# Kernel tuning notes

Hardware: AMD Instinct MI355X
Metric: run time of the kernel (lower is better)

## Reference

```python
import jax, jax.numpy as jnp
from jax import lax
import numpy as np

INPUT_DIM = 64
EMB_DIM = 24   # hardcoded Dense(24) in MyLSTM
UNITS = 128    # hardcoded LSTM_cell(128)


def setup_inputs() -> dict:
    key = jax.random.key(0)
    ks = jax.random.split(key, 12)
    B, T, D = 1024, 2048, INPUT_DIM
    gin = EMB_DIM + UNITS  # 152: concat([x_emb, h])
    s_emb = 1.0 / np.sqrt(D)
    s_g = 1.0 / np.sqrt(gin)
    s_o = 1.0 / np.sqrt(UNITS)
    return {
        "x": jax.random.normal(ks[0], (B, T, D), jnp.float32),
        "W_emb": jax.random.normal(ks[1], (D, EMB_DIM), jnp.float32) * s_emb,
        "b_emb": jnp.zeros((EMB_DIM,), jnp.float32),
        "Wf": jax.random.normal(ks[2], (gin, UNITS), jnp.float32) * s_g,
        "bf": jnp.ones((UNITS,), jnp.float32),  # forget bias init = ones
        "Wi": jax.random.normal(ks[3], (gin, UNITS), jnp.float32) * s_g,
        "bi": jnp.zeros((UNITS,), jnp.float32),
        "Wg": jax.random.normal(ks[4], (gin, UNITS), jnp.float32) * s_g,
        "bg": jnp.zeros((UNITS,), jnp.float32),
        "Wo": jax.random.normal(ks[5], (gin, UNITS), jnp.float32) * s_g,
        "bo": jnp.zeros((UNITS,), jnp.float32),
        "W_out": jax.random.normal(ks[6], (UNITS, 1), jnp.float32) * s_o,
        "b_out": jnp.zeros((1,), jnp.float32),
    }


def reference(x, W_emb, b_emb, Wf, bf, Wi, bi, Wg, bg, Wo, bo, W_out, b_out):
    # embedding: Dense(24, sigmoid) applied per timestep
    e = jax.nn.sigmoid(jnp.einsum("btd,de->bte", x, W_emb) + b_emb)  # [B,T,24]
    B = x.shape[0]
    h0 = jnp.zeros((B, UNITS), x.dtype)
    c0 = jnp.zeros((B, UNITS), x.dtype)

    def step(carry, xt):
        h, c = carry
        z = jnp.concatenate([xt, h], axis=-1)  # [B, 152]
        f = jax.nn.sigmoid(z @ Wf + bf)
        i = jax.nn.sigmoid(z @ Wi + bi)
        g = jnp.tanh(z @ Wg + bg)
        o = jax.nn.sigmoid(z @ Wo + bo)
        c_new = c * f + i * g
        h_new = jnp.tanh(c_new) * o
        return (h_new, c_new), None

    (h_last, _), _ = lax.scan(step, (h0, c0), jnp.swapaxes(e, 0, 1))  # scan over T
    return jax.nn.sigmoid(h_last @ W_out + b_out)  # [B, 1]
```

## Files before the change

kernel.cpp:

```cpp
#include <hip/hip_runtime.h>
#include <hip/hip_bf16.h>

#define T_STEPS 2048
#define BATCH   1024
#define NUNITS  128
#define ROWS    4
#define LOG2E   1.4426950408889634f

typedef __attribute__((ext_vector_type(4))) float  f32x4;
typedef __attribute__((ext_vector_type(2))) int    i32x2;
typedef __attribute__((ext_vector_type(4))) int    int4v;

__device__ __forceinline__ float sigm_pre(float xs) {
    return __builtin_amdgcn_rcpf(1.0f + __builtin_amdgcn_exp2f(-xs));
}
__device__ __forceinline__ float tanh_pre(float xs) {
    return fmaf(-2.0f, __builtin_amdgcn_rcpf(1.0f + __builtin_amdgcn_exp2f(xs)), 1.0f);
}
__device__ __forceinline__ int swap_lo_i(int a, int b) {
    i32x2 r = __builtin_amdgcn_permlane32_swap(a, b, false, false);
    return r[0];
}
__device__ __forceinline__ int swap16_lo_i(int a, int b) {
    i32x2 r = __builtin_amdgcn_permlane16_swap(a, b, false, false);
    return r[0];
}

__global__ __launch_bounds__(256) void emb_kernel(const float* __restrict__ x,
                                                  const float* __restrict__ Wemb,
                                                  const float* __restrict__ bemb,
                                                  uchar* __restrict__ e_out) {
    int g = blockIdx.x * 256 + threadIdx.x;
    int t = g >> 10;
    int b = g & 1023;
    const float* xr = x + ((size_t)b * T_STEPS + t) * 64;

    float4 xv[16];
#pragma unroll
    for (int i = 0; i < 16; i++) xv[i] = ((const float4*)xr)[i];

    float acc[24];
#pragma unroll
    for (int j = 0; j < 24; j++) acc[j] = bemb[j];

#pragma unroll
    for (int d = 0; d < 64; d++) {
        float xs = ((const float*)xv)[d];
#pragma unroll
        for (int j = 0; j < 24; j++) acc[j] = fmaf(xs, Wemb[d * 24 + j], acc[j]);
    }

    uint outp[8] = {0, 0, 0, 0, 0, 0, 0, 0};
#pragma unroll
    for (int j = 0; j < 24; j++) {
        float s = __builtin_amdgcn_rcpf(1.0f + __builtin_amdgcn_exp2f(-LOG2E * acc[j]));
        int q = (int)__builtin_rintf(s * 127.0f);
        outp[j >> 2] |= (uint)(q & 255) << (8 * (j & 3));
    }
    uint4* dst = (uint4*)(e_out + (size_t)g * 32);
    dst[0] = ((const uint4*)outp)[0];
    dst[1] = ((const uint4*)outp)[1];
}

__global__ __launch_bounds__(512, 1) void lstm_kernel(
    const uchar* __restrict__ e_ws,
    const float* __restrict__ Wf, const float* __restrict__ bf_,
    const float* __restrict__ Wi, const float* __restrict__ bi_,
    const float* __restrict__ Wg, const float* __restrict__ bg_,
    const float* __restrict__ Wo, const float* __restrict__ bo_,
    const float* __restrict__ Wout, const float* __restrict__ bout,
    float* __restrict__ out) {
    __shared__ __align__(16) char zq[2][2][4][16][16];

    const int tid  = threadIdx.x;
    const int lane = tid & 63;
    const int wv   = tid >> 6;
    const int l15  = lane & 15;
    const int kg   = lane >> 4;
    const int r0   = blockIdx.x * ROWS;

    const float* Wp[4] = {Wf, Wi, Wg, Wo};
    const float* Bp[4] = {bf_, bi_, bg_, bo_};
    const float gsc[4] = {LOG2E, LOG2E, 2.0f * LOG2E, LOG2E};
    const int ucol = wv * 16 + l15;

    int4v wq[4][3];
    float fct[4], biasv[4];
#pragma unroll
    for (int gt = 0; gt < 4; gt++) {
        float amax = 1e-20f;
        for (int k = 0; k < 152; k++) {
            float v = (k < 128) ? Wp[gt][(24 + k) * NUNITS + ucol]
                                : Wp[gt][(k - 128) * NUNITS + ucol];
            amax = fmaxf(amax, fabsf(v * gsc[gt]));
        }
        float isq = 127.0f / amax;
        fct[gt] = amax * (1.0f / 16129.0f);
#pragma unroll
        for (int ks = 0; ks < 3; ks++) {
#pragma unroll
            for (int w = 0; w < 4; w++) {
                int word = 0;
#pragma unroll
                for (int b = 0; b < 4; b++) {
                    int k = ks * 64 + kg * 16 + w * 4 + b;
                    float v = 0.0f;
                    if (k < 128) v = Wp[gt][(24 + k) * NUNITS + ucol] * gsc[gt];
                    else if (k < 152) v = Wp[gt][(k - 128) * NUNITS + ucol] * gsc[gt];
                    int q = (int)__builtin_rintf(v * isq);
                    word |= (q & 255) << (8 * b);
                }
                wq[gt][ks][w] = word;
            }
        }
        biasv[gt] = Bp[gt][ucol] * gsc[gt];
    }
    const int4v zeroi = {0, 0, 0, 0};

    for (int i = tid; i < (int)(sizeof(zq) / 4); i += 512) ((int*)zq)[i] = 0;

    const char* zrd = &zq[0][0][kg][l15][0];
    char* zwr = &zq[0][ucol >> 6][(ucol >> 4) & 3][kg][ucol & 15];

    const uchar* elbase = e_ws + ((size_t)(r0 + (l15 & 3)) * 32 + kg * 16);
    const bool eload = (kg < 2) && (l15 < 4);
    int4v e0 = zeroi, e1 = zeroi;
    if (eload) {
        e0 = *(const int4v*)(const void*)(elbase);
        e1 = *(const int4v*)(const void*)(elbase + 32768);
    }
    const uchar* eptr = elbase + 2 * 32768;

    __syncthreads();

    float c0 = 0.0f;

    auto STEP = [&](int P, int4v& ecur) {
        int4v acc[4];
#pragma unroll
        for (int gt = 0; gt < 4; gt++)
            acc[gt] = __builtin_amdgcn_mfma_i32_16x16x64_i8(ecur, wq[gt][2], zeroi, 0, 0, 0);

        const char* zb = zrd + P * 2048;
        int4v z0 = *(const int4v*)(const void*)(zb);
        int4v z1 = *(const int4v*)(const void*)(zb + 1024);
#pragma unroll
        for (int gt = 0; gt < 4; gt++)
            acc[gt] = __builtin_amdgcn_mfma_i32_16x16x64_i8(z0, wq[gt][0], acc[gt], 0, 0, 0);
#pragma unroll
        for (int gt = 0; gt < 4; gt++)
            acc[gt] = __builtin_amdgcn_mfma_i32_16x16x64_i8(z1, wq[gt][1], acc[gt], 0, 0, 0);

        if (eload) ecur = *(const int4v*)(const void*)(eptr);
        eptr += 32768;

        float g[4];
#pragma unroll
        for (int gt = 0; gt < 4; gt++) {
            int a0 = swap_lo_i(acc[gt][0], acc[gt][2]);
            int a1 = swap_lo_i(acc[gt][1], acc[gt][3]);
            int sel = swap16_lo_i(a0, a1);
            g[gt] = fmaf((float)sel, fct[gt], biasv[gt]);
        }

        float fg = sigm_pre(g[0]);
        float ig = sigm_pre(g[1]);
        float gg = tanh_pre(g[2]);
        float og = sigm_pre(g[3]);
        c0 = fmaf(c0, fg, ig * gg);
        float h0 = tanh_pre(2.0f * LOG2E * c0) * og;

        int q0i = (int)__builtin_rintf(h0 * 127.0f);
        *(zwr + ((P ^ 1) * 2048)) = (char)q0i;

        asm volatile("s_waitcnt lgkmcnt(0)" ::: "memory");
        __builtin_amdgcn_s_barrier();
        __builtin_amdgcn_sched_barrier(0);
    };

    for (int t = 0; t < T_STEPS; t += 2) {
        STEP(0, e0);
        STEP(1, e1);
    }

    if (tid < ROWS) {
        float s2 = 0.0f;
#pragma unroll
        for (int k = 0; k < NUNITS; k++)
            s2 += (float)zq[0][k >> 6][(k >> 4) & 3][tid][k & 15] * Wout[k];
        float s = s2 * (1.0f / 127.0f) + bout[0];
        out[r0 + tid] = __builtin_amdgcn_rcpf(1.0f + __builtin_amdgcn_exp2f(-LOG2E * s));
    }
}

extern "C" void kernel_launch(void* const* d_in, const int* in_sizes, int n_in,
                              void* d_out, int out_size, void* d_ws, size_t ws_size,
                              hipStream_t stream) {
    const float* x     = (const float*)d_in[0];
    const float* Wemb  = (const float*)d_in[1];
    const float* bemb  = (const float*)d_in[2];
    const float* Wf    = (const float*)d_in[3];
    const float* bf_   = (const float*)d_in[4];
    const float* Wi    = (const float*)d_in[5];
    const float* bi_   = (const float*)d_in[6];
    const float* Wg    = (const float*)d_in[7];
    const float* bg_   = (const float*)d_in[8];
    const float* Wo    = (const float*)d_in[9];
    const float* bo_   = (const float*)d_in[10];
    const float* Wout  = (const float*)d_in[11];
    const float* bout  = (const float*)d_in[12];
    float* out = (float*)d_out;
    uchar* e_ws = (uchar*)d_ws;

    int nrows = BATCH * T_STEPS;
    emb_kernel<<<nrows / 256, 256, 0, stream>>>(x, Wemb, bemb, e_ws);
    lstm_kernel<<<BATCH / ROWS, 512, 0, stream>>>(e_ws, Wf, bf_, Wi, bi_, Wg, bg_,
                                                  Wo, bo_, Wout, bout, out);
}
```

Before: 1.214 ms.

## Run one batch row per single-wave block to eliminate per-step barriers

Each batch row now gets its own single-wave block instead of eight waves sharing four rows. Each lane keeps all 8×4 quantized weight tiles in registers and computes every gate tile itself. The workgroup s_barrier in each recurrent step is gone, and the hidden-state LDS buffer is reduced to single buffering. The cost is about four times more MFMA work per useful row, since only one of the 16 MFMA rows carries real data. It also adds very high register pressure from the 96 int4 weight vectors and leaves fewer waves per CU.

```diff
diff --git a/kernel.cpp b/kernel.cpp
--- a/kernel.cpp
+++ b/kernel.cpp
@@ -4,10 +4,8 @@
 #define T_STEPS 2048
 #define BATCH   1024
 #define NUNITS  128
-#define ROWS    4
 #define LOG2E   1.4426950408889634f
 
-typedef __attribute__((ext_vector_type(4))) float  f32x4;
 typedef __attribute__((ext_vector_type(2))) int    i32x2;
 typedef __attribute__((ext_vector_type(4))) int    int4v;
 
@@ -62,7 +60,7 @@
     dst[1] = ((const uint4*)outp)[1];
 }
 
-__global__ __launch_bounds__(512, 1) void lstm_kernel(
+__global__ __launch_bounds__(64) void lstm_kernel(
     const uchar* __restrict__ e_ws,
     const float* __restrict__ Wf, const float* __restrict__ bf_,
     const float* __restrict__ Wi, const float* __restrict__ bi_,
@@ -70,60 +68,81 @@
     const float* __restrict__ Wo, const float* __restrict__ bo_,
     const float* __restrict__ Wout, const float* __restrict__ bout,
     float* __restrict__ out) {
-    __shared__ __align__(16) char zq[2][2][4][16][16];
-
-    const int tid  = threadIdx.x;
-    const int lane = tid & 63;
-    const int wv   = tid >> 6;
+    __shared__ __align__(16) char zq[2][4][16][16];
+
+    const int lane = threadIdx.x & 63;
     const int l15  = lane & 15;
     const int kg   = lane >> 4;
-    const int r0   = blockIdx.x * ROWS;
+    const int r0   = blockIdx.x;
 
     const float* Wp[4] = {Wf, Wi, Wg, Wo};
     const float* Bp[4] = {bf_, bi_, bg_, bo_};
     const float gsc[4] = {LOG2E, LOG2E, 2.0f * LOG2E, LOG2E};
-    const int ucol = wv * 16 + l15;
-
-    int4v wq[4][3];
-    float fct[4], biasv[4];
-#pragma unroll
-    for (int gt = 0; gt < 4; gt++) {
-        float amax = 1e-20f;
-        for (int k = 0; k < 152; k++) {
-            float v = (k < 128) ? Wp[gt][(24 + k) * NUNITS + ucol]
-                                : Wp[gt][(k - 128) * NUNITS + ucol];
-            amax = fmaxf(amax, fabsf(v * gsc[gt]));
-        }
-        float isq = 127.0f / amax;
-        fct[gt] = amax * (1.0f / 16129.0f);
-#pragma unroll
-        for (int ks = 0; ks < 3; ks++) {
-#pragma unroll
-            for (int w = 0; w < 4; w++) {
-                int word = 0;
-#pragma unroll
-                for (int b = 0; b < 4; b++) {
-                    int k = ks * 64 + kg * 16 + w * 4 + b;
-                    float v = 0.0f;
-                    if (k < 128) v = Wp[gt][(24 + k) * NUNITS + ucol] * gsc[gt];
-                    else if (k < 152) v = Wp[gt][(k - 128) * NUNITS + ucol] * gsc[gt];
-                    int q = (int)__builtin_rintf(v * isq);
-                    word |= (q & 255) << (8 * b);
+
+    const int Ta = (kg & 1) + ((kg >> 1) << 2);
+    const int Tb = Ta + 2;
+    const int ua = Ta * 16 + l15, ub = Tb * 16 + l15;
+
+    int4v wq[8][4][3];
+#pragma unroll
+    for (int T = 0; T < 8; T++) {
+        const int ucol = T * 16 + l15;
+#pragma unroll
+        for (int gt = 0; gt < 4; gt++) {
+            float amax = 1e-20f;
+            for (int k = 0; k < 152; k++) {
+                float v = (k < 128) ? Wp[gt][(24 + k) * NUNITS + ucol]
+                                    : Wp[gt][(k - 128) * NUNITS + ucol];
+                amax = fmaxf(amax, fabsf(v * gsc[gt]));
+            }
+            float isq = 127.0f / amax;
+#pragma unroll
+            for (int ks = 0; ks < 3; ks++) {
+#pragma unroll
+                for (int w = 0; w < 4; w++) {
+                    int word = 0;
+#pragma unroll
+                    for (int b = 0; b < 4; b++) {
+                        int k = ks * 64 + kg * 16 + w * 4 + b;
+                        float v = 0.0f;
+                        if (k < 128) v = Wp[gt][(24 + k) * NUNITS + ucol] * gsc[gt];
+                        else if (k < 152) v = Wp[gt][(k - 128) * NUNITS + ucol] * gsc[gt];
+                        int q = (int)__builtin_rintf(v * isq);
+                        word |= (q & 255) << (8 * b);
+                    }
+                    wq[T][gt][ks][w] = word;
                 }
-                wq[gt][ks][w] = word;
             }
         }
-        biasv[gt] = Bp[gt][ucol] * gsc[gt];
+    }
+    float fct_a[4], fct_b[4], bias_a[4], bias_b[4];
+#pragma unroll
+    for (int gt = 0; gt < 4; gt++) {
+        float ama = 1e-20f, amb = 1e-20f;
+        for (int k = 0; k < 152; k++) {
+            float va = (k < 128) ? Wp[gt][(24 + k) * NUNITS + ua]
+                                 : Wp[gt][(k - 128) * NUNITS + ua];
+            float vb = (k < 128) ? Wp[gt][(24 + k) * NUNITS + ub]
+                                 : Wp[gt][(k - 128) * NUNITS + ub];
+            ama = fmaxf(ama, fabsf(va * gsc[gt]));
+            amb = fmaxf(amb, fabsf(vb * gsc[gt]));
+        }
+        fct_a[gt] = ama * (1.0f / 16129.0f);
+        fct_b[gt] = amb * (1.0f / 16129.0f);
+        bias_a[gt] = Bp[gt][ua] * gsc[gt];
+        bias_b[gt] = Bp[gt][ub] * gsc[gt];
     }
     const int4v zeroi = {0, 0, 0, 0};
 
-    for (int i = tid; i < (int)(sizeof(zq) / 4); i += 512) ((int*)zq)[i] = 0;
-
-    const char* zrd = &zq[0][0][kg][l15][0];
-    char* zwr = &zq[0][ucol >> 6][(ucol >> 4) & 3][kg][ucol & 15];
-
-    const uchar* elbase = e_ws + ((size_t)(r0 + (l15 & 3)) * 32 + kg * 16);
-    const bool eload = (kg < 2) && (l15 < 4);
+    for (int i = lane; i < (int)(sizeof(zq) / 4); i += 64) ((int*)zq)[i] = 0;
+
+    const char* zr0 = &zq[0][kg][l15][0];
+    const char* zr1 = &zq[1][kg][l15][0];
+    char* wa = &zq[ua >> 6][(ua >> 4) & 3][0][ua & 15];
+    char* wb = &zq[ub >> 6][(ub >> 4) & 3][0][ub & 15];
+
+    const uchar* elbase = e_ws + ((size_t)r0 * 32 + kg * 16);
+    const bool eload = (kg < 2) && (l15 == 0);
     int4v e0 = zeroi, e1 = zeroi;
     if (eload) {
         e0 = *(const int4v*)(const void*)(elbase);
@@ -133,63 +152,67 @@
 
     __syncthreads();
 
-    float c0 = 0.0f;
-
-    auto STEP = [&](int P, int4v& ecur) {
-        int4v acc[4];
-#pragma unroll
-        for (int gt = 0; gt < 4; gt++)
-            acc[gt] = __builtin_amdgcn_mfma_i32_16x16x64_i8(ecur, wq[gt][2], zeroi, 0, 0, 0);
-
-        const char* zb = zrd + P * 2048;
-        int4v z0 = *(const int4v*)(const void*)(zb);
-        int4v z1 = *(const int4v*)(const void*)(zb + 1024);
-#pragma unroll
-        for (int gt = 0; gt < 4; gt++)
-            acc[gt] = __builtin_amdgcn_mfma_i32_16x16x64_i8(z0, wq[gt][0], acc[gt], 0, 0, 0);
-#pragma unroll
-        for (int gt = 0; gt < 4; gt++)
-            acc[gt] = __builtin_amdgcn_mfma_i32_16x16x64_i8(z1, wq[gt][1], acc[gt], 0, 0, 0);
+    float ca = 0.0f, cb = 0.0f;
+
+    auto STEP = [&](int4v& ecur) {
+        int4v z0 = *(const int4v*)(const void*)(zr0);
+        int4v z1 = *(const int4v*)(const void*)(zr1);
+
+        float gA[4], gB[4];
+#pragma unroll
+        for (int gt = 0; gt < 4; gt++) {
+            int4v acc[8];
+#pragma unroll
+            for (int T = 0; T < 8; T++)
+                acc[T] = __builtin_amdgcn_mfma_i32_16x16x64_i8(ecur, wq[T][gt][2], zeroi, 0, 0, 0);
+#pragma unroll
+            for (int T = 0; T < 8; T++)
+                acc[T] = __builtin_amdgcn_mfma_i32_16x16x64_i8(z0, wq[T][gt][0], acc[T], 0, 0, 0);
+#pragma unroll
+            for (int T = 0; T < 8; T++)
+                acc[T] = __builtin_amdgcn_mfma_i32_16x16x64_i8(z1, wq[T][gt][1], acc[T], 0, 0, 0);
+
+            int s0 = swap_lo_i(acc[0][0], acc[4][0]);
+            int s1 = swap_lo_i(acc[1][0], acc[5][0]);
+            int s2 = swap_lo_i(acc[2][0], acc[6][0]);
+            int s3 = swap_lo_i(acc[3][0], acc[7][0]);
+            int va = swap16_lo_i(s0, s1);
+            int vb = swap16_lo_i(s2, s3);
+            gA[gt] = fmaf((float)va, fct_a[gt], bias_a[gt]);
+            gB[gt] = fmaf((float)vb, fct_b[gt], bias_b[gt]);
+        }
 
         if (eload) ecur = *(const int4v*)(const void*)(eptr);
         eptr += 32768;
 
-        float g[4];
-#pragma unroll
-        for (int gt = 0; gt < 4; gt++) {
-            int a0 = swap_lo_i(acc[gt][0], acc[gt][2]);
-            int a1 = swap_lo_i(acc[gt][1], acc[gt][3]);
-            int sel = swap16_lo_i(a0, a1);
-            g[gt] = fmaf((float)sel, fct[gt], biasv[gt]);
-        }
-
-        float fg = sigm_pre(g[0]);
-        float ig = sigm_pre(g[1]);
-        float gg = tanh_pre(g[2]);
-        float og = sigm_pre(g[3]);
-        c0 = fmaf(c0, fg, ig * gg);
-        float h0 = tanh_pre(2.0f * LOG2E * c0) * og;
-
-        int q0i = (int)__builtin_rintf(h0 * 127.0f);
-        *(zwr + ((P ^ 1) * 2048)) = (char)q0i;
+        float fga = sigm_pre(gA[0]), fgb = sigm_pre(gB[0]);
+        float iga = sigm_pre(gA[1]), igb = sigm_pre(gB[1]);
+        float gga = tanh_pre(gA[2]), ggb = tanh_pre(gB[2]);
+        float oga = sigm_pre(gA[3]), ogb = sigm_pre(gB[3]);
+        ca = fmaf(ca, fga, iga * gga);
+        cb = fmaf(cb, fgb, igb * ggb);
+        float ha = tanh_pre(2.0f * LOG2E * ca) * oga;
+        float hb = tanh_pre(2.0f * LOG2E * cb) * ogb;
+
+        *wa = (char)(int)__builtin_rintf(ha * 127.0f);
+        *wb = (char)(int)__builtin_rintf(hb * 127.0f);
 
         asm volatile("s_waitcnt lgkmcnt(0)" ::: "memory");
-        __builtin_amdgcn_s_barrier();
         __builtin_amdgcn_sched_barrier(0);
     };
 
     for (int t = 0; t < T_STEPS; t += 2) {
-        STEP(0, e0);
-        STEP(1, e1);
-    }
-
-    if (tid < ROWS) {
+        STEP(e0);
+        STEP(e1);
+    }
+
+    if (lane == 0) {
         float s2 = 0.0f;
 #pragma unroll
         for (int k = 0; k < NUNITS; k++)
-            s2 += (float)zq[0][k >> 6][(k >> 4) & 3][tid][k & 15] * Wout[k];
+            s2 += (float)zq[k >> 6][(k >> 4) & 3][0][k & 15] * Wout[k];
         float s = s2 * (1.0f / 127.0f) + bout[0];
-        out[r0 + tid] = __builtin_amdgcn_rcpf(1.0f + __builtin_amdgcn_exp2f(-LOG2E * s));
+        out[r0] = __builtin_amdgcn_rcpf(1.0f + __builtin_amdgcn_exp2f(-LOG2E * s));
     }
 }
 
@@ -214,6 +237,6 @@
 
     int nrows = BATCH * T_STEPS;
     emb_kernel<<<nrows / 256, 256, 0, stream>>>(x, Wemb, bemb, e_ws);
-    lstm_kernel<<<BATCH / ROWS, 512, 0, stream>>>(e_ws, Wf, bf_, Wi, bi_, Wg, bg_,
-                                                  Wo, bo_, Wout, bout, out);
-}
+    lstm_kernel<<<BATCH, 64, 0, stream>>>(e_ws, Wf, bf_, Wi, bi_, Wg, bg_,
+                                          Wo, bo_, Wout, bout, out);
+}
```

After: 3.912 ms. 3.22x slower.
